# Kernel optimization log

Hardware: AMD Instinct MI355X
Metric: run time of the kernel (lower is better)

Reference implementation:

```python
import jax, jax.numpy as jnp
import numpy as np

VOCAB, D, B, T = 32000, 1024, 4, 2048

def setup_inputs() -> dict:
    key = jax.random.key(0)
    ks = jax.random.split(key, 7)
    std = 0.01  # model initializes all weights with std=0.01
    return {
        "x": jax.random.randint(ks[0], (B, T), 0, VOCAB),
        "emb_w": jax.random.normal(ks[1], (VOCAB, D), jnp.float32) * std,
        "wq": jax.random.normal(ks[2], (D, D), jnp.float32) * std,
        "wk": jax.random.normal(ks[3], (D, D), jnp.float32) * std,
        "wv": jax.random.normal(ks[4], (D, D), jnp.float32) * std,
        "wo": jax.random.normal(ks[5], (D, D), jnp.float32) * std,
        "wout": jax.random.normal(ks[6], (VOCAB, D), jnp.float32) * std,
    }

def fhe_act(x):
    # polynomial activation: 0.1*x^2 + 0.1*x
    return x * x * 0.1 + x * 0.1

def reference(x, emb_w, wq, wk, wv, wo, wout):
    h = emb_w[x] * 0.01                                 # [B,T,D]
    q = (h @ wq.T) * 0.01                               # [B,T,D]
    k = (h @ wk.T) * 0.01                               # [B,T,D]
    v = (h @ wv.T) * 0.1                                # [B,T,D]
    attn = jnp.einsum('btd,bsd->bts', q, k) * 0.01      # [B,T,T] full (no causal mask)
    attn = fhe_act(attn)
    out = jnp.einsum('bts,bsd->btd', attn, v) * 0.01    # [B,T,D]
    out = (out @ wo.T) * 0.1                            # [B,T,D]
    logits = out @ wout.T                               # [B,T,VOCAB]
    return logits
```

## Files before the change

kernel.cpp:

```cpp
#include <hip/hip_runtime.h>


typedef __bf16 bf16_t;
typedef __bf16 bf16x8 __attribute__((ext_vector_type(8)));
typedef __bf16 bf16x4 __attribute__((ext_vector_type(4)));
typedef float  f32x4  __attribute__((ext_vector_type(4)));

#define VOCAB 32000
#define DIM   1024
#define BATCH 4
#define SEQ   2048
#define BT    (BATCH*SEQ)

__device__ __forceinline__ void gload_lds16(const void* g, void* l) {
    __builtin_amdgcn_global_load_lds(
        (const __attribute__((address_space(1))) void*)g,
        (__attribute__((address_space(3))) void*)l,
        16, 0, 0);
}

__global__ void cast_f32_to_bf16(const float* __restrict__ in, bf16_t* __restrict__ out, int n4) {
    int i = blockIdx.x * blockDim.x + threadIdx.x;
    if (i < n4) {
        float4 v = ((const float4*)in)[i];
        bf16x4 o;
        o.x = (bf16_t)v.x; o.y = (bf16_t)v.y; o.z = (bf16_t)v.z; o.w = (bf16_t)v.w;
        ((bf16x4*)out)[i] = o;
    }
}

__global__ void embed_gather(const int* __restrict__ x, const float* __restrict__ emb,
                             bf16_t* __restrict__ h) {
    const int tok = blockIdx.x;
    const int row = x[tok];
    const float4* src = (const float4*)(emb + (long)row * DIM);
    bf16x4* dst = (bf16x4*)(h + (long)tok * DIM);
    int j = threadIdx.x;
    float4 v = src[j];
    bf16x4 o;
    o.x = (bf16_t)(v.x * 0.01f); o.y = (bf16_t)(v.y * 0.01f);
    o.z = (bf16_t)(v.z * 0.01f); o.w = (bf16_t)(v.w * 0.01f);
    dst[j] = o;
}

template<int ACT, typename CT>
__global__ __launch_bounds__(256) void gemm_bt(
    const bf16_t* __restrict__ A, const bf16_t* __restrict__ B, CT* __restrict__ C,
    int M, int N, int K, long sA, long sB, long sC, float scale)
{
    __shared__ __align__(16) bf16_t lsA[128 * 32];
    __shared__ __align__(16) bf16_t lsB[128 * 32];

    const int bz = blockIdx.z;
    A += (long)bz * sA;  B += (long)bz * sB;  C += (long)bz * sC;

    const int tm = blockIdx.y, tn = blockIdx.x;
    const int t = threadIdx.x;
    const int lane = t & 63, wave = t >> 6;
    const int wm = (wave >> 1) * 64;
    const int wn = (wave & 1) * 64;

    const int srow = t >> 2;
    const int scol = (t & 3) * 8;
    const bf16_t* gA = A + (long)(tm * 128 + srow) * K + scol;
    const bf16_t* gB = B + (long)(tn * 128 + srow) * K + scol;
    bf16_t* lA = &lsA[srow * 32 + scol];
    bf16_t* lB = &lsB[srow * 32 + scol];

    f32x4 acc[4][4];
#pragma unroll
    for (int i = 0; i < 4; ++i)
#pragma unroll
        for (int j = 0; j < 4; ++j)
            acc[i][j] = (f32x4){0.f, 0.f, 0.f, 0.f};

    const int arow = lane & 15;
    const int acol = (lane >> 4) * 8;

    for (int k0 = 0; k0 < K; k0 += 32) {
        __syncthreads();
        gload_lds16(gA + k0,                lA);
        gload_lds16(gA + k0 + 64 * (long)K, lA + 64 * 32);
        gload_lds16(gB + k0,                lB);
        gload_lds16(gB + k0 + 64 * (long)K, lB + 64 * 32);
        __syncthreads();

        bf16x8 af[4], bfr[4];
#pragma unroll
        for (int i = 0; i < 4; ++i) {
            af[i]  = *(const bf16x8*)&lsA[(wm + i * 16 + arow) * 32 + acol];
            bfr[i] = *(const bf16x8*)&lsB[(wn + i * 16 + arow) * 32 + acol];
        }
#pragma unroll
        for (int i = 0; i < 4; ++i)
#pragma unroll
            for (int j = 0; j < 4; ++j)
                acc[i][j] = __builtin_amdgcn_mfma_f32_16x16x32_bf16(af[i], bfr[j], acc[i][j], 0, 0, 0);
    }

    const int crow0 = tm * 128 + wm + (lane >> 4) * 4;
    const int ccol0 = tn * 128 + wn + (lane & 15);
#pragma unroll
    for (int i = 0; i < 4; ++i)
#pragma unroll
        for (int j = 0; j < 4; ++j)
#pragma unroll
            for (int r = 0; r < 4; ++r) {
                float s = acc[i][j][r] * scale;
                if (ACT) s = s * s * 0.1f + s * 0.1f;
                C[(long)(crow0 + i * 16 + r) * N + (ccol0 + j * 16)] = (CT)s;
            }
}

template<int ACT, int SWZ, typename CT>
__global__ __launch_bounds__(512, 2) void gemm_bt_256(
    const bf16_t* __restrict__ A, const bf16_t* __restrict__ B, CT* __restrict__ C,
    int N, int K, long sA, long sB, long sC, float scale)
{
    __shared__ __align__(16) char smem[131072];
    char* const sm = smem;

    const int bz = blockIdx.z;
    A += (long)bz * sA;  B += (long)bz * sB;  C += (long)bz * sC;

    const int lin = blockIdx.x;
    int tm, tn;
    if (SWZ == 0) { const int xcd = lin & 7, jj = lin >> 3; tm = xcd * 4 + (jj & 3); tn = jj >> 2; }
    else          { tm = lin & 7; tn = lin >> 3; }
    const long trow0 = (long)tm * 256, tcol0 = (long)tn * 256;

    const int tid  = threadIdx.x;
    const int lane = tid & 63;
    const int wave = tid >> 6;
    const int wm = wave >> 2;
    const int wn = wave & 3;
    const int lr = lane & 15;
    const int ko2 = (lane >> 4) * 16;
    const int rbase = lr * 64 + (ko2 ^ (((lr >> 1) & 3) << 4));

    const int o0 = tid * 16, o1 = 8192 + tid * 16;
    int sr0, sc0, sr1, sc1;
    {
        int ol = o0 ^ (((o0 >> 7) & 3) << 4);
        sr0 = ((ol >> 10) >> 1) * 16 + ((ol >> 6) & 15);
        sc0 = ((ol >> 10) & 1) * 32 + ((ol & 63) >> 1);
        ol = o1 ^ (((o1 >> 7) & 3) << 4);
        sr1 = ((ol >> 10) >> 1) * 16 + ((ol >> 6) & 15);
        sc1 = ((ol >> 10) & 1) * 32 + ((ol & 63) >> 1);
    }

    const bf16_t* Abase = A + trow0 * K;
    const bf16_t* Bbase = B + tcol0 * K;

#define STAGE_HT(gbase, kt, half, ldsh) do {                                          \
    gload_lds16((gbase) + (long)((half) * 128 + sr0) * K + ((kt) * 64 + sc0), (ldsh) + o0); \
    gload_lds16((gbase) + (long)((half) * 128 + sr1) * K + ((kt) * 64 + sc1), (ldsh) + o1); \
} while (0)

    f32x4 acc[8][4];
#pragma unroll
    for (int i = 0; i < 8; ++i)
#pragma unroll
        for (int j = 0; j < 4; ++j)
            acc[i][j] = (f32x4){0.f, 0.f, 0.f, 0.f};

#define PHASE_LO(ks, ...) do {                                                        \
    bf16x8 af_[4];                                                                    \
    af_[0] = *(const bf16x8*)(ldsA + ((wm * 4 + 0) * 2 + (ks)) * 1024 + rbase);       \
    _Pragma("unroll")                                                                 \
    for (int c_ = 0; c_ < 4; ++c_)                                                    \
        bv_[c_] = *(const bf16x8*)(ldsB + (c_ >> 1) * 16384 +                         \
                      ((wn * 2 + (c_ & 1)) * 2 + (ks)) * 1024 + rbase);               \
    _Pragma("unroll")                                                                 \
    for (int i_ = 1; i_ < 4; ++i_)                                                    \
        af_[i_] = *(const bf16x8*)(ldsA +                                             \
                      ((wm * 4 + i_) * 2 + (ks)) * 1024 + rbase);                     \
    __VA_ARGS__;                                                                      \
    __builtin_amdgcn_s_setprio(1);                                                    \
    _Pragma("unroll")                                                                 \
    for (int i_ = 0; i_ < 4; ++i_)                                                    \
        _Pragma("unroll")                                                             \
        for (int c_ = 0; c_ < 4; ++c_)                                                \
            acc[i_][c_] = __builtin_amdgcn_mfma_f32_16x16x32_bf16(                    \
                af_[i_], bv_[c_], acc[i_][c_], 0, 0, 0);                              \
    __builtin_amdgcn_s_setprio(0);                                                    \
    __builtin_amdgcn_sched_barrier(0);                                                \
    asm volatile("s_barrier" ::: "memory");                                           \
} while (0)

#define PHASE_HI(ks, ...) do {                                                        \
    bf16x8 af_[4];                                                                    \
    _Pragma("unroll")                                                                 \
    for (int i_ = 0; i_ < 4; ++i_)                                                    \
        af_[i_] = *(const bf16x8*)(ldsA + 16384 +                                     \
                      ((wm * 4 + i_) * 2 + (ks)) * 1024 + rbase);                     \
    __VA_ARGS__;                                                                      \
    __builtin_amdgcn_s_setprio(1);                                                    \
    _Pragma("unroll")                                                                 \
    for (int i_ = 0; i_ < 4; ++i_)                                                    \
        _Pragma("unroll")                                                             \
        for (int c_ = 0; c_ < 4; ++c_)                                                \
            acc[4 + i_][c_] = __builtin_amdgcn_mfma_f32_16x16x32_bf16(                \
                af_[i_], bv_[c_], acc[4 + i_][c_], 0, 0, 0);                          \
    __builtin_amdgcn_s_setprio(0);                                                    \
    __builtin_amdgcn_sched_barrier(0);                                                \
} while (0)

    {
        char* a0 = sm;
        char* b0 = sm + 32768;
        char* a1 = sm + 65536;
        char* b1 = sm + 65536 + 32768;
        STAGE_HT(Abase, 0, 0, a0);
        STAGE_HT(Bbase, 0, 0, b0);
        STAGE_HT(Abase, 0, 1, a0 + 16384);
        STAGE_HT(Bbase, 0, 1, b0 + 16384);
        STAGE_HT(Abase, 1, 0, a1);
        STAGE_HT(Bbase, 1, 0, b1);
        asm volatile("s_waitcnt vmcnt(4)" ::: "memory");
        asm volatile("s_barrier" ::: "memory");
    }

    const int NT = K / 64;
    for (int t = 0; t < NT; ++t) {
        const int buf = t & 1;
        char* ldsA  = sm + buf * 65536;
        char* ldsB  = ldsA + 32768;
        char* ldsAn = sm + (buf ^ 1) * 65536;
        char* ldsBn = ldsAn + 32768;
        bf16x8 bv_[4];

        PHASE_LO(0,
              if (t + 1 < NT) {
                  STAGE_HT(Abase, t + 1, 1, ldsAn + 16384);
                  STAGE_HT(Bbase, t + 1, 1, ldsBn + 16384);
              });

        PHASE_HI(0, );
        asm volatile("s_barrier" ::: "memory");

        PHASE_LO(1, );

        PHASE_HI(1,
              if (t + 2 < NT) {
                  STAGE_HT(Abase, t + 2, 0, ldsA);
                  STAGE_HT(Bbase, t + 2, 0, ldsB);
              });
        if (t + 2 < NT) { asm volatile("s_waitcnt vmcnt(4)" ::: "memory"); }
        else            { asm volatile("s_waitcnt vmcnt(0)" ::: "memory"); }
        asm volatile("s_barrier" ::: "memory");
    }

    const int erow = (lane >> 4) * 4;
    const int ecol = lane & 15;
#pragma unroll
    for (int a = 0; a < 8; ++a)
#pragma unroll
        for (int c = 0; c < 4; ++c)
#pragma unroll
            for (int r = 0; r < 4; ++r) {
                long row = trow0 + (a >> 2) * 128 + wm * 64 + (a & 3) * 16 + erow + r;
                long col = tcol0 + (c >> 1) * 128 + wn * 32 + (c & 1) * 16 + ecol;
                float s = acc[a][c][r] * scale;
                if (ACT) s = s * s * 0.1f + s * 0.1f;
                C[row * N + col] = (CT)s;
            }
#undef PHASE_LO
#undef PHASE_HI
#undef STAGE_HT
}

extern "C" void kernel_launch(void* const* d_in, const int* in_sizes, int n_in,
                              void* d_out, int out_size, void* d_ws, size_t ws_size,
                              hipStream_t stream) {
    const int*   x    = (const int*)d_in[0];
    const float* emb  = (const float*)d_in[1];
    const float* wq   = (const float*)d_in[2];
    const float* wk   = (const float*)d_in[3];
    const float* wv   = (const float*)d_in[4];
    const float* wo   = (const float*)d_in[5];
    const float* wout = (const float*)d_in[6];
    float* logits = (float*)d_out;

    char* ws = (char*)d_ws;
    size_t off = 0;
    auto alloc = [&](size_t bytes) {
        char* p = ws + off;
        off += (bytes + 255) & ~(size_t)255;
        return p;
    };
    bf16_t* hb    = (bf16_t*)alloc((size_t)BT * DIM * 2);
    bf16_t* qb    = (bf16_t*)alloc((size_t)BT * DIM * 2);
    bf16_t* kb    = (bf16_t*)alloc((size_t)BT * DIM * 2);
    bf16_t* vtb   = (bf16_t*)alloc((size_t)BATCH * DIM * SEQ * 2);
    bf16_t* attnb = (bf16_t*)alloc((size_t)BATCH * SEQ * SEQ * 2);
    bf16_t* o1b   = (bf16_t*)alloc((size_t)BT * DIM * 2);
    bf16_t* o2b   = (bf16_t*)alloc((size_t)BT * DIM * 2);
    bf16_t* wqb   = (bf16_t*)alloc((size_t)DIM * DIM * 2);
    bf16_t* wkb   = (bf16_t*)alloc((size_t)DIM * DIM * 2);
    bf16_t* wvb   = (bf16_t*)alloc((size_t)DIM * DIM * 2);
    bf16_t* wob   = (bf16_t*)alloc((size_t)DIM * DIM * 2);
    bf16_t* woutb = (bf16_t*)alloc((size_t)VOCAB * DIM * 2);

    {
        int n4 = DIM * DIM / 4;
        cast_f32_to_bf16<<<n4 / 256, 256, 0, stream>>>(wq, wqb, n4);
        cast_f32_to_bf16<<<n4 / 256, 256, 0, stream>>>(wk, wkb, n4);
        cast_f32_to_bf16<<<n4 / 256, 256, 0, stream>>>(wv, wvb, n4);
        cast_f32_to_bf16<<<n4 / 256, 256, 0, stream>>>(wo, wob, n4);
        int n4o = VOCAB * DIM / 4;
        cast_f32_to_bf16<<<n4o / 256, 256, 0, stream>>>(wout, woutb, n4o);
    }

    embed_gather<<<BT, 256, 0, stream>>>(x, emb, hb);

    dim3 blk(256);
    gemm_bt<0, bf16_t><<<dim3(DIM / 128, BT / 128, 1), blk, 0, stream>>>(
        hb, wqb, qb, BT, DIM, DIM, 0, 0, 0, 0.01f);
    gemm_bt<0, bf16_t><<<dim3(DIM / 128, BT / 128, 1), blk, 0, stream>>>(
        hb, wkb, kb, BT, DIM, DIM, 0, 0, 0, 0.01f);
    gemm_bt<0, bf16_t><<<dim3(SEQ / 128, DIM / 128, BATCH), blk, 0, stream>>>(
        wvb, hb, vtb, DIM, SEQ, DIM, 0, (long)SEQ * DIM, (long)DIM * SEQ, 0.1f);

    gemm_bt_256<1, 1, bf16_t><<<dim3(64, 1, BATCH), 512, 0, stream>>>(
        qb, kb, attnb, SEQ, DIM,
        (long)SEQ * DIM, (long)SEQ * DIM, (long)SEQ * SEQ, 0.01f);

    gemm_bt<0, bf16_t><<<dim3(DIM / 128, SEQ / 128, BATCH), blk, 0, stream>>>(
        attnb, vtb, o1b, SEQ, DIM, SEQ,
        (long)SEQ * SEQ, (long)DIM * SEQ, (long)SEQ * DIM, 0.01f);
    gemm_bt<0, bf16_t><<<dim3(DIM / 128, BT / 128, 1), blk, 0, stream>>>(
        o1b, wob, o2b, BT, DIM, DIM, 0, 0, 0, 0.1f);

    gemm_bt_256<0, 0, float><<<dim3((BT / 256) * (VOCAB / 256), 1, 1), 512, 0, stream>>>(
        o2b, woutb, logits, VOCAB, DIM, 0, 0, 0, 1.0f);
}
```

Before: 921.3 us.

## Fuse Q/K projections and add 256x128 GEMM kernel for projection and logits

New measurement: 906.9 us. Within noise of the previous version (-1.6%).

```diff
diff --git a/kernel.cpp b/kernel.cpp
--- a/kernel.cpp
+++ b/kernel.cpp
@@ -115,7 +115,7 @@
 template<int ACT, int SWZ, typename CT>
 __global__ __launch_bounds__(512, 2) void gemm_bt_256(
     const bf16_t* __restrict__ A, const bf16_t* __restrict__ B, CT* __restrict__ C,
-    int N, int K, long sA, long sB, long sC, float scale)
+    int N, int K, int lda, int ldb, long sA, long sB, long sC, float scale)
 {
     __shared__ __align__(16) char smem[131072];
     char* const sm = smem;
@@ -149,12 +149,12 @@
         sc1 = ((ol >> 10) & 1) * 32 + ((ol & 63) >> 1);
     }
 
-    const bf16_t* Abase = A + trow0 * K;
-    const bf16_t* Bbase = B + tcol0 * K;
-
-#define STAGE_HT(gbase, kt, half, ldsh) do {                                          \
-    gload_lds16((gbase) + (long)((half) * 128 + sr0) * K + ((kt) * 64 + sc0), (ldsh) + o0); \
-    gload_lds16((gbase) + (long)((half) * 128 + sr1) * K + ((kt) * 64 + sc1), (ldsh) + o1); \
+    const bf16_t* Abase = A + trow0 * lda;
+    const bf16_t* Bbase = B + tcol0 * ldb;
+
+#define STAGE_HT(gbase, ld, kt, half, ldsh) do {                                      \
+    gload_lds16((gbase) + (long)((half) * 128 + sr0) * (ld) + ((kt) * 64 + sc0), (ldsh) + o0); \
+    gload_lds16((gbase) + (long)((half) * 128 + sr1) * (ld) + ((kt) * 64 + sc1), (ldsh) + o1); \
 } while (0)
 
     f32x4 acc[8][4];
@@ -211,12 +211,12 @@
         char* b0 = sm + 32768;
         char* a1 = sm + 65536;
         char* b1 = sm + 65536 + 32768;
-        STAGE_HT(Abase, 0, 0, a0);
-        STAGE_HT(Bbase, 0, 0, b0);
-        STAGE_HT(Abase, 0, 1, a0 + 16384);
-        STAGE_HT(Bbase, 0, 1, b0 + 16384);
-        STAGE_HT(Abase, 1, 0, a1);
-        STAGE_HT(Bbase, 1, 0, b1);
+        STAGE_HT(Abase, lda, 0, 0, a0);
+        STAGE_HT(Bbase, ldb, 0, 0, b0);
+        STAGE_HT(Abase, lda, 0, 1, a0 + 16384);
+        STAGE_HT(Bbase, ldb, 0, 1, b0 + 16384);
+        STAGE_HT(Abase, lda, 1, 0, a1);
+        STAGE_HT(Bbase, ldb, 1, 0, b1);
         asm volatile("s_waitcnt vmcnt(4)" ::: "memory");
         asm volatile("s_barrier" ::: "memory");
     }
@@ -232,19 +232,16 @@
 
         PHASE_LO(0,
               if (t + 1 < NT) {
-                  STAGE_HT(Abase, t + 1, 1, ldsAn + 16384);
-                  STAGE_HT(Bbase, t + 1, 1, ldsBn + 16384);
+                  STAGE_HT(Abase, lda, t + 1, 1, ldsAn + 16384);
+                  STAGE_HT(Bbase, ldb, t + 1, 1, ldsBn + 16384);
               });
-
         PHASE_HI(0, );
         asm volatile("s_barrier" ::: "memory");
-
         PHASE_LO(1, );
-
         PHASE_HI(1,
               if (t + 2 < NT) {
-                  STAGE_HT(Abase, t + 2, 0, ldsA);
-                  STAGE_HT(Bbase, t + 2, 0, ldsB);
+                  STAGE_HT(Abase, lda, t + 2, 0, ldsA);
+                  STAGE_HT(Bbase, ldb, t + 2, 0, ldsB);
               });
         if (t + 2 < NT) { asm volatile("s_waitcnt vmcnt(4)" ::: "memory"); }
         else            { asm volatile("s_waitcnt vmcnt(0)" ::: "memory"); }
@@ -268,6 +265,121 @@
 #undef PHASE_LO
 #undef PHASE_HI
 #undef STAGE_HT
+}
+
+template<int ACT, int SWZ, typename CT>
+__global__ __launch_bounds__(512, 4) void gemm_bt_256x128(
+    const bf16_t* __restrict__ A, const bf16_t* __restrict__ B, CT* __restrict__ C,
+    int N, int K, long sA, long sB, long sC, float scale)
+{
+    __shared__ __align__(16) char smem[2 * 24576];
+    char* const sm = smem;
+
+    const int bz = blockIdx.z;
+    A += (long)bz * sA;  B += (long)bz * sB;  C += (long)bz * sC;
+
+    const int lin = blockIdx.x;
+    int tm, tn;
+    if (SWZ == 0) { const int xcd = lin & 7, jj = lin >> 3; tm = xcd * 4 + (jj & 3); tn = jj >> 2; }
+    else          { tm = lin & 7; tn = lin >> 3; }
+    const long trow0 = (long)tm * 256, tcol0 = (long)tn * 128;
+
+    const int tid  = threadIdx.x;
+    const int lane = tid & 63;
+    const int wave = tid >> 6;
+    const int wm = wave >> 1;
+    const int wn = wave & 1;
+    const int lr = lane & 15;
+    const int ko2 = (lane >> 4) * 16;
+    const int rbase = lr * 64 + (ko2 ^ (((lr >> 1) & 3) << 4));
+
+    const int o0 = tid * 16;
+    const int ol = o0 ^ (((o0 >> 7) & 3) << 4);
+    const int sr = (ol >> 10) * 16 + ((ol >> 6) & 15);
+    const int sc = (ol & 63) >> 1;
+
+    const bf16_t* Abase = A + trow0 * K;
+    const bf16_t* Bbase = B + tcol0 * K;
+
+#define STAGE_A(kt, bufp) do {                                                        \
+    gload_lds16(Abase + (long)sr * K         + ((kt) * 32 + sc), (bufp) + o0);        \
+    gload_lds16(Abase + (long)(128 + sr) * K + ((kt) * 32 + sc), (bufp) + 8192 + o0); \
+} while (0)
+#define STAGE_B(kt, bufp) do {                                                        \
+    gload_lds16(Bbase + (long)sr * K + ((kt) * 32 + sc), (bufp) + 16384 + o0);        \
+} while (0)
+
+    f32x4 acc[4][4];
+#pragma unroll
+    for (int i = 0; i < 4; ++i)
+#pragma unroll
+        for (int j = 0; j < 4; ++j)
+            acc[i][j] = (f32x4){0.f, 0.f, 0.f, 0.f};
+
+#define BAR() asm volatile("s_barrier" ::: "memory")
+
+    STAGE_A(0, sm);
+    STAGE_B(0, sm);
+    STAGE_A(1, sm + 24576);
+    asm volatile("s_waitcnt vmcnt(2)" ::: "memory");
+    BAR();
+
+    const int NT = K / 32;
+    for (int t = 0; t < NT; ++t) {
+        char* cur = sm + (t & 1) * 24576;
+        char* idl = sm + ((t & 1) ^ 1) * 24576;
+
+        bf16x8 af_[4], bvA[2], bvB[2];
+        af_[0] = *(const bf16x8*)(cur + (wm * 4 + 0) * 1024 + rbase);
+        bvA[0] = *(const bf16x8*)(cur + 16384 + (wn * 2 + 0) * 1024 + rbase);
+        bvA[1] = *(const bf16x8*)(cur + 16384 + (wn * 2 + 1) * 1024 + rbase);
+#pragma unroll
+        for (int i = 1; i < 4; ++i)
+            af_[i] = *(const bf16x8*)(cur + (wm * 4 + i) * 1024 + rbase);
+        if (t + 1 < NT) STAGE_B(t + 1, idl);
+        __builtin_amdgcn_s_setprio(1);
+#pragma unroll
+        for (int i = 0; i < 4; ++i) {
+            acc[i][0] = __builtin_amdgcn_mfma_f32_16x16x32_bf16(af_[i], bvA[0], acc[i][0], 0, 0, 0);
+            acc[i][1] = __builtin_amdgcn_mfma_f32_16x16x32_bf16(af_[i], bvA[1], acc[i][1], 0, 0, 0);
+        }
+        __builtin_amdgcn_s_setprio(0);
+        __builtin_amdgcn_sched_barrier(0);
+        BAR();
+
+        bvB[0] = *(const bf16x8*)(cur + 16384 + (4 + wn * 2 + 0) * 1024 + rbase);
+        bvB[1] = *(const bf16x8*)(cur + 16384 + (4 + wn * 2 + 1) * 1024 + rbase);
+        if (t + 2 < NT) STAGE_A(t + 2, cur);
+        __builtin_amdgcn_s_setprio(1);
+#pragma unroll
+        for (int i = 0; i < 4; ++i) {
+            acc[i][2] = __builtin_amdgcn_mfma_f32_16x16x32_bf16(af_[i], bvB[0], acc[i][2], 0, 0, 0);
+            acc[i][3] = __builtin_amdgcn_mfma_f32_16x16x32_bf16(af_[i], bvB[1], acc[i][3], 0, 0, 0);
+        }
+        __builtin_amdgcn_s_setprio(0);
+        __builtin_amdgcn_sched_barrier(0);
+        if (t + 2 < NT) { asm volatile("s_waitcnt vmcnt(2)" ::: "memory"); }
+        else            { asm volatile("s_waitcnt vmcnt(0)" ::: "memory"); }
+        BAR();
+    }
+
+    const int erow = (lane >> 4) * 4;
+    const int ecol = lane & 15;
+#pragma unroll
+    for (int i = 0; i < 4; ++i)
+#pragma unroll
+        for (int j = 0; j < 4; ++j)
+#pragma unroll
+            for (int r = 0; r < 4; ++r) {
+                long row = trow0 + wm * 64 + i * 16 + erow + r;
+                long col = tcol0 + (j >> 1) * 64 + wn * 32 + (j & 1) * 16 + ecol;
+                float s = acc[i][j][r] * scale;
+                if (ACT) s = s * s * 0.1f + s * 0.1f;
+                C[row * N + col] = (CT)s;
+            }
+#undef STAGE_A
+#undef STAGE_B
+#undef BAR
 }
 
 extern "C" void kernel_launch(void* const* d_in, const int* in_sizes, int n_in,
@@ -290,22 +402,20 @@
         return p;
     };
     bf16_t* hb    = (bf16_t*)alloc((size_t)BT * DIM * 2);
-    bf16_t* qb    = (bf16_t*)alloc((size_t)BT * DIM * 2);
-    bf16_t* kb    = (bf16_t*)alloc((size_t)BT * DIM * 2);
+    bf16_t* qkb   = (bf16_t*)alloc((size_t)BT * 2 * DIM * 2);
     bf16_t* vtb   = (bf16_t*)alloc((size_t)BATCH * DIM * SEQ * 2);
     bf16_t* attnb = (bf16_t*)alloc((size_t)BATCH * SEQ * SEQ * 2);
     bf16_t* o1b   = (bf16_t*)alloc((size_t)BT * DIM * 2);
     bf16_t* o2b   = (bf16_t*)alloc((size_t)BT * DIM * 2);
-    bf16_t* wqb   = (bf16_t*)alloc((size_t)DIM * DIM * 2);
-    bf16_t* wkb   = (bf16_t*)alloc((size_t)DIM * DIM * 2);
+    bf16_t* wqkb  = (bf16_t*)alloc((size_t)2 * DIM * DIM * 2);
     bf16_t* wvb   = (bf16_t*)alloc((size_t)DIM * DIM * 2);
     bf16_t* wob   = (bf16_t*)alloc((size_t)DIM * DIM * 2);
     bf16_t* woutb = (bf16_t*)alloc((size_t)VOCAB * DIM * 2);
 
     {
         int n4 = DIM * DIM / 4;
-        cast_f32_to_bf16<<<n4 / 256, 256, 0, stream>>>(wq, wqb, n4);
-        cast_f32_to_bf16<<<n4 / 256, 256, 0, stream>>>(wk, wkb, n4);
+        cast_f32_to_bf16<<<n4 / 256, 256, 0, stream>>>(wq, wqkb, n4);
+        cast_f32_to_bf16<<<n4 / 256, 256, 0, stream>>>(wk, wqkb + (size_t)DIM * DIM, n4);
         cast_f32_to_bf16<<<n4 / 256, 256, 0, stream>>>(wv, wvb, n4);
         cast_f32_to_bf16<<<n4 / 256, 256, 0, stream>>>(wo, wob, n4);
         int n4o = VOCAB * DIM / 4;
@@ -315,16 +425,15 @@
     embed_gather<<<BT, 256, 0, stream>>>(x, emb, hb);
 
     dim3 blk(256);
-    gemm_bt<0, bf16_t><<<dim3(DIM / 128, BT / 128, 1), blk, 0, stream>>>(
-        hb, wqb, qb, BT, DIM, DIM, 0, 0, 0, 0.01f);
-    gemm_bt<0, bf16_t><<<dim3(DIM / 128, BT / 128, 1), blk, 0, stream>>>(
-        hb, wkb, kb, BT, DIM, DIM, 0, 0, 0, 0.01f);
+    gemm_bt_256x128<0, 0, bf16_t><<<dim3((BT / 256) * (2 * DIM / 128), 1, 1), 512, 0, stream>>>(
+        hb, wqkb, qkb, 2 * DIM, DIM, 0, 0, 0, 0.01f);
+
     gemm_bt<0, bf16_t><<<dim3(SEQ / 128, DIM / 128, BATCH), blk, 0, stream>>>(
         wvb, hb, vtb, DIM, SEQ, DIM, 0, (long)SEQ * DIM, (long)DIM * SEQ, 0.1f);
 
     gemm_bt_256<1, 1, bf16_t><<<dim3(64, 1, BATCH), 512, 0, stream>>>(
-        qb, kb, attnb, SEQ, DIM,
-        (long)SEQ * DIM, (long)SEQ * DIM, (long)SEQ * SEQ, 0.01f);
+        qkb, qkb + DIM, attnb, SEQ, DIM, 2 * DIM, 2 * DIM,
+        (long)SEQ * 2 * DIM, (long)SEQ * 2 * DIM, (long)SEQ * SEQ, 0.01f);
 
     gemm_bt<0, bf16_t><<<dim3(DIM / 128, SEQ / 128, BATCH), blk, 0, stream>>>(
         attnb, vtb, o1b, SEQ, DIM, SEQ,
@@ -332,6 +441,6 @@
     gemm_bt<0, bf16_t><<<dim3(DIM / 128, BT / 128, 1), blk, 0, stream>>>(
         o1b, wob, o2b, BT, DIM, DIM, 0, 0, 0, 0.1f);
 
-    gemm_bt_256<0, 0, float><<<dim3((BT / 256) * (VOCAB / 256), 1, 1), 512, 0, stream>>>(
+    gemm_bt_256x128<0, 0, float><<<dim3((BT / 256) * (VOCAB / 128), 1, 1), 512, 0, stream>>>(
         o2b, woutb, logits, VOCAB, DIM, 0, 0, 0, 1.0f);
 }
```
